# Performance work log

Measured on AMD Instinct MI355X. Metric: run time of the kernel, lower is better.

## Reference

```python
import jax, jax.numpy as jnp
import numpy as np

HID = 512      # hidden_dim
HEADS = 8
DK = HID // HEADS   # 64
WIN = 128      # sliding window (attend to self + previous 128)
TYPE_V = 157
TYPE_D = 192
CONCAT = TYPE_D + 128 + 128 + 128  # 576


def _ln(x, g, b):
    m = jnp.mean(x, -1, keepdims=True)
    v = jnp.mean((x - m) ** 2, -1, keepdims=True)
    return (x - m) * jax.lax.rsqrt(v + 1e-5) * g + b


def _rope(t):
    # interleaved rotary embedding (rotary_embedding_torch default), t: [B,H,L,D]
    d, L = t.shape[-1], t.shape[-2]
    inv = 1.0 / (10000.0 ** (jnp.arange(0, d, 2, dtype=jnp.float32) / d))
    ang = jnp.arange(L, dtype=jnp.float32)[:, None] * inv  # [L, d/2]
    c, s = jnp.cos(ang), jnp.sin(ang)
    x1, x2 = t[..., 0::2], t[..., 1::2]
    return jnp.stack([x1 * c - x2 * s, x1 * s + x2 * c], -1).reshape(t.shape)


def _forward(emb, reg_w, reg_b, br_w, br_b, mem_w, mem_b, inst_w, inst_b,
             ln1_g, ln1_b, qkv_w, outp_w, outp_b, ln2_g, ln2_b, head_w, head_b, x):
    # --- InstructionEncoder ---
    tid = x[..., 0]
    reg = x[..., 1:65].astype(jnp.float32)
    mem = x[..., 65:129].astype(jnp.float32)
    br = x[..., 129:161].astype(jnp.float32)
    cat = jnp.concatenate([
        emb[tid],
        reg @ reg_w.T + reg_b,
        br @ br_w.T + br_b,
        mem @ mem_w.T + mem_b,
    ], -1)
    cat = jax.nn.silu(cat)
    h = jax.nn.silu(_ln(cat @ inst_w.T + inst_b, ln1_g, ln1_b))  # [B,L,HID]

    # --- MultiHeadSelfAttention (banded causal window) ---
    B, L, _ = h.shape
    # torch rearrange '... l (h d c) -> c ... h l d': last dim factors (h, d, 3)
    qkv = (h @ qkv_w.T).reshape(B, L, HEADS, DK, 3)
    q = jnp.transpose(qkv[..., 0], (0, 2, 1, 3))  # [B,H,L,D]
    k = jnp.transpose(qkv[..., 1], (0, 2, 1, 3))
    v = jnp.transpose(qkv[..., 2], (0, 2, 1, 3))
    q = _rope(q)
    k = _rope(k)

    nb = L // WIN
    qb = q.reshape(B, HEADS, nb, WIN, DK)
    kb = k.reshape(B, HEADS, nb, WIN, DK)
    vb = v.reshape(B, HEADS, nb, WIN, DK)
    # each query block attends to its own block and the previous one
    kprev = jnp.pad(kb, ((0, 0), (0, 0), (1, 0), (0, 0), (0, 0)))[:, :, :nb]
    vprev = jnp.pad(vb, ((0, 0), (0, 0), (1, 0), (0, 0), (0, 0)))[:, :, :nb]
    kc = jnp.concatenate([kprev, kb], 3)  # [B,H,nb,2W,D]
    vc = jnp.concatenate([vprev, vb], 3)
    sc = jnp.einsum('bhnqd,bhnkd->bhnqk', qb, kc) / np.sqrt(DK).astype(np.float32)
    qi = jnp.arange(WIN)[:, None]
    kj = jnp.arange(2 * WIN)[None, :]
    rel = (WIN + qi) - kj                      # query_pos - key_pos within band
    allowed = (rel >= 0) & (rel <= WIN)        # causal, window = 128 back
    valid = (kj[None] >= WIN) | (jnp.arange(nb)[:, None, None] > 0)  # no prev block for block 0
    mask = allowed[None] & valid               # [nb, W, 2W]
    sc = jnp.where(mask, sc, jnp.finfo(sc.dtype).min)
    p = jax.nn.softmax(sc, -1)
    o = jnp.einsum('bhnqk,bhnkd->bhnqd', p, vc).reshape(B, HEADS, L, DK)
    o = jnp.transpose(o, (0, 2, 1, 3)).reshape(B, L, HID)
    attn = o @ outp_w.T + outp_b

    # --- MultiTaskOutputHead ---
    y = jax.nn.silu(_ln(attn, ln2_g, ln2_b))
    out = y @ head_w.T + head_b  # [B,L,9]
    fetch = jax.nn.softplus(out[..., 0])
    exec_c = jax.nn.softplus(out[..., 1])
    bm = jax.nn.sigmoid(out[..., 2])
    tlb = jax.nn.sigmoid(out[..., 3])
    ic = jax.nn.sigmoid(out[..., 4])
    dc = jax.nn.softmax(out[..., 5:9], -1)
    return jnp.concatenate([fetch[..., None], exec_c[..., None], bm[..., None],
                            tlb[..., None], ic[..., None], dc], -1)


def setup_inputs():
    key = jax.random.key(0)
    ks = jax.random.split(key, 12)
    B, L = 4, 8192

    def w(k, shape, fan):
        return jax.random.normal(k, shape, jnp.float32) / np.sqrt(fan).astype(np.float32)

    inp = {}
    inp['emb'] = jax.random.normal(ks[0], (TYPE_V, TYPE_D), jnp.float32)
    inp['reg_w'] = w(ks[1], (128, 64), 64); inp['reg_b'] = jnp.zeros((128,), jnp.float32)
    inp['br_w'] = w(ks[2], (128, 32), 32); inp['br_b'] = jnp.zeros((128,), jnp.float32)
    inp['mem_w'] = w(ks[3], (128, 64), 64); inp['mem_b'] = jnp.zeros((128,), jnp.float32)
    inp['inst_w'] = w(ks[4], (HID, CONCAT), CONCAT); inp['inst_b'] = jnp.zeros((HID,), jnp.float32)
    inp['ln1_g'] = jnp.ones((HID,), jnp.float32); inp['ln1_b'] = jnp.zeros((HID,), jnp.float32)
    inp['qkv_w'] = w(ks[5], (3 * HID, HID), HID)
    inp['outp_w'] = w(ks[6], (HID, HID), HID); inp['outp_b'] = jnp.zeros((HID,), jnp.float32)
    inp['ln2_g'] = jnp.ones((HID,), jnp.float32); inp['ln2_b'] = jnp.zeros((HID,), jnp.float32)
    inp['head_w'] = w(ks[7], (9, HID), HID); inp['head_b'] = jnp.zeros((9,), jnp.float32)
    tid = jax.random.randint(ks[8], (B, L, 1), 0, TYPE_V)
    feats = jax.random.randint(ks[9], (B, L, 160), 0, 2)
    inp['x'] = jnp.concatenate([tid, feats], -1).astype(jnp.int32)
    return inp


def reference(emb, reg_w, reg_b, br_w, br_b, mem_w, mem_b, inst_w, inst_b,
              ln1_g, ln1_b, qkv_w, outp_w, outp_b, ln2_g, ln2_b, head_w, head_b, x):
    return _forward(emb, reg_w, reg_b, br_w, br_b, mem_w, mem_b, inst_w, inst_b,
                    ln1_g, ln1_b, qkv_w, outp_w, outp_b, ln2_g, ln2_b, head_w, head_b, x)
```

## Files before the change

### kernel.cpp

```cpp
#include <hip/hip_runtime.h>
#include <hip/hip_bf16.h>
#include <math.h>
#include <type_traits>

#define LSEQ 8192
#define BATCH 4
#define M_TOK (BATCH * LSEQ)

typedef __attribute__((ext_vector_type(8))) short bf16x8;
typedef __attribute__((ext_vector_type(4))) float f32x4;
typedef __attribute__((ext_vector_type(16))) float f32x16;

__device__ __forceinline__ float siluf(float x) {
  return x / (1.f + __expf(-x));
}

__device__ __forceinline__ float bf2f(uint u16) {
  union { float f; uint u; } c;
  c.u = u16 << 16;
  return c.f;
}

__device__ __forceinline__ uint cvtpk_bf16(float lo, float hi) {
  uint r;
  asm volatile("v_cvt_pk_bf16_f32 %0, %1, %2" : "=v"(r) : "v"(lo), "v"(hi));
  return r;
}

__device__ __forceinline__ void perm32swap(uint& a, uint& b) {
  asm volatile("v_permlane32_swap_b32 %0, %1" : "+v"(a), "+v"(b));
}

__device__ __forceinline__ void gload16(const ushort* g, short* l) {
  __builtin_amdgcn_global_load_lds(
      (const __attribute__((address_space(1))) void*)g,
      (__attribute__((address_space(3))) void*)l, 16, 0, 0);
}

#define NW1 (512 * 576)
#define NW3 (512 * 512)
#define NW2 (1536 * 512)
#define NW4 (384 * 192)
#define NTAB (8192 * 32)

__global__ __launch_bounds__(256) void setup_kernel(
    const float* __restrict__ inst_w, const float* __restrict__ outp_w,
    const float* __restrict__ qkv_w, const float* __restrict__ reg_w,
    const float* __restrict__ reg_b, const float* __restrict__ br_w,
    const float* __restrict__ br_b, const float* __restrict__ mem_w,
    const float* __restrict__ mem_b, __hip_bfloat16* __restrict__ w16,
    float2* __restrict__ tab) {
  int i = blockIdx.x * 256 + threadIdx.x;
  if (i < NW1) {
    w16[i] = __float2bfloat16(inst_w[i]);
    return;
  }
  i -= NW1;
  if (i < NW3) {
    w16[NW1 + i] = __float2bfloat16(outp_w[i]);
    return;
  }
  i -= NW3;
  if (i < NW2) {
    int np = i / 512, k = i % 512;
    int which = np >> 9, rem = np & 511;
    int h = rem >> 6, d = rem & 63;
    int n = h * 192 + d * 3 + which;
    w16[NW1 + NW3 + i] = __float2bfloat16(qkv_w[n * 512 + k]);
    return;
  }
  i -= NW2;
  if (i < NW4) {
    int o = i / 192, c = i % 192;
    float v = 0.f;
    if (o < 128) {
      if (c == 0) v = reg_b[o];
      else if (c <= 64) v = reg_w[o * 64 + (c - 1)];
    } else if (o < 256) {
      int oo = o - 128;
      if (c == 0) v = br_b[oo];
      else if (c >= 129 && c <= 160) v = br_w[oo * 32 + (c - 129)];
    } else {
      int oo = o - 256;
      if (c == 0) v = mem_b[oo];
      else if (c >= 65 && c <= 128) v = mem_w[oo * 64 + (c - 65)];
    }
    w16[NW1 + NW3 + NW2 + i] = __float2bfloat16(v);
    return;
  }
  i -= NW4;
  if (i < NTAB) {
    int pos = i >> 5, p = i & 31;
    float inv = expf(-(float)p * 0.28782313662f);
    float sn, cs;
    sincosf((float)pos * inv, &sn, &cs);
    tab[i] = make_float2(cs, sn);
  }
}

__global__ __launch_bounds__(256) void prep_kernel(
    const int* __restrict__ x, const float* __restrict__ emb,
    __hip_bfloat16* __restrict__ cat, __hip_bfloat16* __restrict__ Fb) {
  int gid = blockIdx.x * 256 + threadIdx.x;
  int t = gid / 48;
  int g = gid % 48;
  if (t >= M_TOK) return;
  const int* xr = x + (size_t)t * 161;
  union { __hip_bfloat16 h[8]; uint4 u; } pk;
  if (g < 24) {
    int c0 = g * 8;
    const float* e = emb + xr[0] * 192 + c0;
#pragma unroll
    for (int j = 0; j < 8; ++j) pk.h[j] = __float2bfloat16(siluf(e[j]));
    *(uint4*)&cat[(size_t)t * 576 + c0] = pk.u;
  } else {
    int c0 = (g - 24) * 8;
#pragma unroll
    for (int j = 0; j < 8; ++j) {
      int c = c0 + j;
      float v = (c == 0) ? 1.f : ((c <= 160) ? (float)xr[c] : 0.f);
      pk.h[j] = __float2bfloat16(v);
    }
    *(uint4*)&Fb[(size_t)t * 192 + c0] = pk.u;
  }
}

template <typename OT, bool SILU = false>
__global__ __launch_bounds__(256) void gemm_mfma(
    const ushort* __restrict__ A, const ushort* __restrict__ W,
    const float* __restrict__ bias, OT* __restrict__ C, int M, int N, int K,
    int ldc, int ntn) {
  __shared__ __align__(16) short As[2][128 * 32];
  __shared__ __align__(16) short Bs[2][128 * 32];
  const int tid = threadIdx.x;
  const int lane = tid & 63;
  const int wid = tid >> 6;
  const int wr = wid >> 1, wc = wid & 1;
  const int nwg = gridDim.x;
  const int orig = blockIdx.x;
  const int qq = nwg >> 3, rr = nwg & 7;
  const int xcd = orig & 7;
  const int wgid = (xcd < rr ? xcd * (qq + 1) : rr * (qq + 1) + (xcd - rr) * qq)
                   + (orig >> 3);
  const int row0 = (wgid / ntn) * 128, col0 = (wgid % ntn) * 128;

  const int lrow = lane >> 2;
  const int lch = (lane & 3) * 8;
  const int frow = lane & 15;
  const int fk = (lane >> 4) * 8;

  const ushort* Abase = A + (size_t)(row0 + 32 * wid + lrow) * K + lch;
  const ushort* Wbase = W + (size_t)(col0 + 32 * wid + lrow) * K + lch;
  short* Al[2] = {&As[0][32 * wid * 32], &As[1][32 * wid * 32]};
  short* Bl[2] = {&Bs[0][32 * wid * 32], &Bs[1][32 * wid * 32]};

  f32x4 acc[4][4];
  const f32x4 z = {0.f, 0.f, 0.f, 0.f};
#pragma unroll
  for (int i = 0; i < 4; ++i)
#pragma unroll
    for (int j = 0; j < 4; ++j) acc[i][j] = z;

  const int T = K >> 5;
  gload16(Abase, Al[0]);
  gload16(Abase + (size_t)16 * K, Al[0] + 512);
  gload16(Wbase, Bl[0]);
  gload16(Wbase + (size_t)16 * K, Bl[0] + 512);

  for (int t = 0; t < T; ++t) {
    __syncthreads();
    if (t + 1 < T) {
      const ushort* An = Abase + (t + 1) * 32;
      const ushort* Wn = Wbase + (t + 1) * 32;
      short* Ad = Al[(t + 1) & 1];
      short* Bd = Bl[(t + 1) & 1];
      gload16(An, Ad);
      gload16(An + (size_t)16 * K, Ad + 512);
      gload16(Wn, Bd);
      gload16(Wn + (size_t)16 * K, Bd + 512);
    }
    const short* Ab = As[t & 1];
    const short* Bb = Bs[t & 1];
    bf16x8 af[4], bfr[4];
#pragma unroll
    for (int i = 0; i < 4; ++i)
      af[i] = *(const bf16x8*)&Ab[(wr * 64 + i * 16 + frow) * 32 + fk];
#pragma unroll
    for (int j = 0; j < 4; ++j)
      bfr[j] = *(const bf16x8*)&Bb[(wc * 64 + j * 16 + frow) * 32 + fk];
#pragma unroll
    for (int i = 0; i < 4; ++i)
#pragma unroll
      for (int j = 0; j < 4; ++j)
        acc[i][j] = __builtin_amdgcn_mfma_f32_16x16x32_bf16(af[i], bfr[j],
                                                            acc[i][j], 0, 0, 0);
  }

  const int crow0 = row0 + wr * 64 + (lane >> 4) * 4;
  const int ccol0 = col0 + wc * 64 + (lane & 15);
#pragma unroll
  for (int j = 0; j < 4; ++j) {
    const int col = ccol0 + j * 16;
    const float bv = bias ? bias[col] : 0.f;
#pragma unroll
    for (int i = 0; i < 4; ++i) {
#pragma unroll
      for (int r = 0; r < 4; ++r) {
        float v = acc[i][j][r] + bv;
        if constexpr (SILU) v = siluf(v);
        size_t off = (size_t)(crow0 + i * 16 + r) * ldc + col;
        if constexpr (std::is_same<OT, float>::value) {
          C[off] = v;
        } else {
          C[off] = __float2bfloat16(v);
        }
      }
    }
  }
}

template <bool HEAD>
__global__ __launch_bounds__(512, 2) void gemm_ln_fused(
    const ushort* __restrict__ A, const ushort* __restrict__ W,
    const float* __restrict__ bias, const float* __restrict__ g,
    const float* __restrict__ b2, const float* __restrict__ hw,
    const float* __restrict__ hb, __hip_bfloat16* __restrict__ C,
    float* __restrict__ out, int K) {
  __shared__ __align__(16) short As[2][128 * 32];
  __shared__ __align__(16) short Bs[2][512 * 32];
  __shared__ float rs[4][128], rss[4][128];
  __shared__ float o9[4][128][9];
  const int tid = threadIdx.x;
  const int lane = tid & 63;
  const int wid = tid >> 6;
  const int wr = wid & 1, wc = wid >> 1;
  const int row0 = blockIdx.x * 128;
  const int frow = lane & 15;
  const int fk = (lane >> 4) * 8;

  const ushort* Abase =
      A + (size_t)(row0 + 16 * wid + (lane >> 2)) * K + (lane & 3) * 8;
  const ushort* Wbase = W + (size_t)(64 * wid + (lane >> 2)) * K + (lane & 3) * 8;
  short* Adst[2] = {&As[0][16 * wid * 32], &As[1][16 * wid * 32]};
  short* Bdst[2] = {&Bs[0][64 * wid * 32], &Bs[1][64 * wid * 32]};

  f32x4 acc[4][8];
  const f32x4 z = {0.f, 0.f, 0.f, 0.f};
#pragma unroll
  for (int i = 0; i < 4; ++i)
#pragma unroll
    for (int j = 0; j < 8; ++j) acc[i][j] = z;

  const int T = K >> 5;
  gload16(Abase, Adst[0]);
#pragma unroll
  for (int q = 0; q < 4; ++q)
    gload16(Wbase + (size_t)q * 16 * K, Bdst[0] + q * 16 * 32);

  for (int t = 0; t < T; ++t) {
    __syncthreads();
    if (t + 1 < T) {
      const ushort* An = Abase + (t + 1) * 32;
      const ushort* Wn = Wbase + (t + 1) * 32;
      short* Ad = Adst[(t + 1) & 1];
      short* Bd = Bdst[(t + 1) & 1];
      gload16(An, Ad);
#pragma unroll
      for (int q = 0; q < 4; ++q)
        gload16(Wn + (size_t)q * 16 * K, Bd + q * 16 * 32);
    }
    const short* Ab = As[t & 1];
    const short* Bb = Bs[t & 1];
    bf16x8 af[4], bfr[8];
#pragma unroll
    for (int i = 0; i < 4; ++i)
      af[i] = *(const bf16x8*)&Ab[(wr * 64 + i * 16 + frow) * 32 + fk];
#pragma unroll
    for (int j = 0; j < 8; ++j)
      bfr[j] = *(const bf16x8*)&Bb[(wc * 128 + j * 16 + frow) * 32 + fk];
#pragma unroll
    for (int i = 0; i < 4; ++i)
#pragma unroll
      for (int j = 0; j < 8; ++j)
        acc[i][j] = __builtin_amdgcn_mfma_f32_16x16x32_bf16(af[i], bfr[j],
                                                            acc[i][j], 0, 0, 0);
  }

  float bv[8], gv[8], b2v[8];
#pragma unroll
  for (int j = 0; j < 8; ++j) {
    int col = wc * 128 + (lane & 15) + j * 16;
    bv[j] = bias[col];
    gv[j] = g[col];
    b2v[j] = b2[col];
  }
  float sum_[4][4], sq_[4][4];
#pragma unroll
  for (int i = 0; i < 4; ++i)
#pragma unroll
    for (int r = 0; r < 4; ++r) { sum_[i][r] = 0.f; sq_[i][r] = 0.f; }
#pragma unroll
  for (int i = 0; i < 4; ++i)
#pragma unroll
    for (int j = 0; j < 8; ++j)
#pragma unroll
      for (int r = 0; r < 4; ++r) {
        float v = acc[i][j][r] + bv[j];
        acc[i][j][r] = v;
        sum_[i][r] += v;
        sq_[i][r] += v * v;
      }
#pragma unroll
  for (int i = 0; i < 4; ++i)
#pragma unroll
    for (int r = 0; r < 4; ++r)
#pragma unroll
      for (int off = 1; off < 16; off <<= 1) {
        sum_[i][r] += __shfl_xor(sum_[i][r], off, 64);
        sq_[i][r] += __shfl_xor(sq_[i][r], off, 64);
      }
  if ((lane & 15) == 0) {
#pragma unroll
    for (int i = 0; i < 4; ++i)
#pragma unroll
      for (int r = 0; r < 4; ++r) {
        int lr = wr * 64 + (lane >> 4) * 4 + i * 16 + r;
        rs[wc][lr] = sum_[i][r];
        rss[wc][lr] = sq_[i][r];
      }
  }
  __syncthreads();
#pragma unroll
  for (int i = 0; i < 4; ++i)
#pragma unroll
    for (int r = 0; r < 4; ++r) {
      int lr = wr * 64 + (lane >> 4) * 4 + i * 16 + r;
      float S = rs[0][lr] + rs[1][lr] + rs[2][lr] + rs[3][lr];
      float SS = rss[0][lr] + rss[1][lr] + rss[2][lr] + rss[3][lr];
      float mean = S * (1.f / 512.f);
      float var = SS * (1.f / 512.f) - mean * mean;
      float rstd = rsqrtf(var + 1e-5f);
#pragma unroll
      for (int j = 0; j < 8; ++j) {
        float y = (acc[i][j][r] - mean) * rstd * gv[j] + b2v[j];
        acc[i][j][r] = siluf(y);
      }
    }

  if constexpr (!HEAD) {
#pragma unroll
    for (int i = 0; i < 4; ++i)
#pragma unroll
      for (int r = 0; r < 4; ++r) {
        int grow = row0 + wr * 64 + (lane >> 4) * 4 + i * 16 + r;
#pragma unroll
        for (int j = 0; j < 8; ++j)
          C[(size_t)grow * 512 + wc * 128 + (lane & 15) + j * 16] =
              __float2bfloat16(acc[i][j][r]);
      }
  } else {
#pragma unroll
    for (int r9 = 0; r9 < 9; ++r9) {
      float hw8[8];
#pragma unroll
      for (int j = 0; j < 8; ++j)
        hw8[j] = hw[r9 * 512 + wc * 128 + (lane & 15) + j * 16];
      float pacc[4][4];
#pragma unroll
      for (int i = 0; i < 4; ++i)
#pragma unroll
        for (int r = 0; r < 4; ++r) {
          float p = 0.f;
#pragma unroll
          for (int j = 0; j < 8; ++j) p = fmaf(acc[i][j][r], hw8[j], p);
#pragma unroll
          for (int off = 1; off < 16; off <<= 1) p += __shfl_xor(p, off, 64);
          pacc[i][r] = p;
        }
      if ((lane & 15) == 0) {
#pragma unroll
        for (int i = 0; i < 4; ++i)
#pragma unroll
          for (int r = 0; r < 4; ++r) {
            int lr = wr * 64 + (lane >> 4) * 4 + i * 16 + r;
            o9[wc][lr][r9] = pacc[i][r];
          }
      }
    }
    __syncthreads();
    if (tid < 128) {
      float raw[9];
#pragma unroll
      for (int r9 = 0; r9 < 9; ++r9)
        raw[r9] = o9[0][tid][r9] + o9[1][tid][r9] + o9[2][tid][r9] +
                  o9[3][tid][r9] + hb[r9];
      float* op = out + (size_t)(row0 + tid) * 9;
      op[0] = fmaxf(raw[0], 0.f) + log1pf(expf(-fabsf(raw[0])));
      op[1] = fmaxf(raw[1], 0.f) + log1pf(expf(-fabsf(raw[1])));
      op[2] = 1.f / (1.f + expf(-raw[2]));
      op[3] = 1.f / (1.f + expf(-raw[3]));
      op[4] = 1.f / (1.f + expf(-raw[4]));
      float mx = fmaxf(fmaxf(raw[5], raw[6]), fmaxf(raw[7], raw[8]));
      float e0 = expf(raw[5] - mx), e1 = expf(raw[6] - mx);
      float e2 = expf(raw[7] - mx), e3 = expf(raw[8] - mx);
      float inv = 1.f / (e0 + e1 + e2 + e3);
      op[5] = e0 * inv; op[6] = e1 * inv; op[7] = e2 * inv; op[8] = e3 * inv;
    }
  }
}

__global__ __launch_bounds__(256) void attn_kernel(
    const __hip_bfloat16* __restrict__ qkv, const float2* __restrict__ tab,
    __hip_bfloat16* __restrict__ o_out) {
  __shared__ __align__(16) short Kc[2][64 * 72];
  __shared__ __align__(16) short Vt[2][64 * 72];
  __shared__ __align__(16) float rbuf[4][32];
  const int blk = blockIdx.x;
  const int nbIdx = blk & 63;
  const int h = (blk >> 6) & 7;
  const int b = blk >> 9;
  const int tid = threadIdx.x;
  const int w = tid >> 6;
  const int lane = tid & 63;
  const int lq = lane & 31;
  const int hi = lane >> 5;
  const size_t seqBase = (size_t)b * LSEQ;
  const int qi = w * 32 + lq;
  const int qtok = nbIdx * 128 + qi;

  const ushort* qkvu = (const ushort*)qkv;

  bf16x8 qf[4];
  {
    const ushort* Qrow = qkvu + (seqBase + qtok) * 1536 + h * 64;
#pragma unroll
    for (int s = 0; s < 4; ++s) {
      int dim0 = 16 * s + 8 * hi;
      bf16x8 qv = *(const bf16x8*)(Qrow + dim0);
      const float4* tp = (const float4*)(tab + qtok * 32 + dim0 / 2);
      float4 t01 = tp[0], t23 = tp[1];
      float cs[4] = {t01.x, t01.z, t23.x, t23.z};
      float sn[4] = {t01.y, t01.w, t23.y, t23.w};
      union { uint u[4]; bf16x8 v; } pk;
#pragma unroll
      for (int j = 0; j < 4; ++j) {
        float x1 = bf2f((ushort)qv[2 * j]);
        float x2 = bf2f((ushort)qv[2 * j + 1]);
        float r0 = (x1 * cs[j] - x2 * sn[j]) * 0.125f;
        float r1 = (x1 * sn[j] + x2 * cs[j]) * 0.125f;
        pk.u[j] = cvtpk_bf16(r0, r1);
      }
      qf[s] = pk.v;
    }
  }

  const f32x16 Z16 = {0.f};
  f32x16 oa0 = Z16, oa1 = Z16;
  float m0 = -3.0e38f, l = 0.f;

  const int cstart = (nbIdx == 0) ? 2 : 0;
  const int cw0 = (w >= 2) ? 1 : 0;
  const int cw1 = (w >= 2) ? 3 : 2;

  const int skk = tid >> 2;
  const int sd0 = (tid & 3) * 16;

  bf16x8 kreg0, kreg1, vreg0, vreg1;

  auto issue = [&](int c) {
    int ktok = (nbIdx - 1) * 128 + c * 64 + skk;
    const ushort* base = qkvu + (seqBase + ktok) * 1536 + h * 64 + sd0;
    kreg0 = *(const bf16x8*)(base + 512);
    kreg1 = *(const bf16x8*)(base + 512 + 8);
    vreg0 = *(const bf16x8*)(base + 1024);
    vreg1 = *(const bf16x8*)(base + 1024 + 8);
  };

  auto write_chunk = [&](int c) {
    short* Kb = Kc[c & 1];
    short* Vb = Vt[c & 1];
    int ktok = (nbIdx - 1) * 128 + c * 64 + skk;
    const float4* tp = (const float4*)(tab + ktok * 32 + (sd0 >> 1));
    float4 t0 = tp[0], t1 = tp[1], t2 = tp[2], t3 = tp[3];
    const int swk = ((skk >> 3) & 3) << 5;
    {
      float cs[4] = {t0.x, t0.z, t1.x, t1.z};
      float sn[4] = {t0.y, t0.w, t1.y, t1.w};
      union { uint u[4]; bf16x8 v; } pk;
#pragma unroll
      for (int j = 0; j < 4; ++j) {
        float x1 = bf2f((ushort)kreg0[2 * j]);
        float x2 = bf2f((ushort)kreg0[2 * j + 1]);
        pk.u[j] = cvtpk_bf16(x1 * cs[j] - x2 * sn[j], x1 * sn[j] + x2 * cs[j]);
      }
      *(bf16x8*)((char*)Kb + skk * 144 + ((sd0 * 2) ^ swk)) = pk.v;
    }
    {
      float cs[4] = {t2.x, t2.z, t3.x, t3.z};
      float sn[4] = {t2.y, t2.w, t3.y, t3.w};
      union { uint u[4]; bf16x8 v; } pk;
#pragma unroll
      for (int j = 0; j < 4; ++j) {
        float x1 = bf2f((ushort)kreg1[2 * j]);
        float x2 = bf2f((ushort)kreg1[2 * j + 1]);
        pk.u[j] = cvtpk_bf16(x1 * cs[j] - x2 * sn[j], x1 * sn[j] + x2 * cs[j]);
      }
      *(bf16x8*)((char*)Kb + skk * 144 + (((sd0 + 8) * 2) ^ swk)) = pk.v;
    }
#pragma unroll
    for (int j = 0; j < 8; ++j) {
      int d0 = sd0 + j;
      *(short*)((char*)Vb + d0 * 144 +
                ((skk * 2) ^ (((d0 >> 4) & 3) << 5))) = vreg0[j];
      int d1 = sd0 + 8 + j;
      *(short*)((char*)Vb + d1 * 144 +
                ((skk * 2) ^ (((d1 >> 4) & 3) << 5))) = vreg1[j];
    }
  };

  issue(cstart);
  write_chunk(cstart);

  for (int c = cstart; c < 4; ++c) {
    if (c < 3) issue(c + 1);
    __syncthreads();
    if (c >= cw0 && c <= cw1) {
      const char* Kb = (const char*)Kc[c & 1];
      const char* Vb = (const char*)Vt[c & 1];

      bf16x8 ka[2][4];
#pragma unroll
      for (int t2 = 0; t2 < 2; ++t2)
#pragma unroll
        for (int s = 0; s < 4; ++s) {
          int kk = 32 * t2 + lq;
          int byteoff =
              kk * 144 + ((32 * s + 16 * hi) ^ (((kk >> 3) & 3) << 5));
          ka[t2][s] = *(const bf16x8*)(Kb + byteoff);
        }
      f32x16 st0 = Z16, st1 = Z16;
#pragma unroll
      for (int s = 0; s < 4; ++s) {
        st0 = __builtin_amdgcn_mfma_f32_32x32x16_bf16(ka[0][s], qf[s], st0, 0, 0, 0);
        st1 = __builtin_amdgcn_mfma_f32_32x32x16_bf16(ka[1][s], qf[s], st1, 0, 0, 0);
      }

      float p2[2][16];
      float pmax = -3.0e38f;
#pragma unroll
      for (int t2 = 0; t2 < 2; ++t2)
#pragma unroll
        for (int r = 0; r < 16; ++r) {
          int key = c * 64 + 32 * t2 + (r & 3) + 8 * (r >> 2) + 4 * hi;
          float sv = (t2 ? st1[r] : st0[r]);
          bool act = (key >= qi) && (key <= qi + 128);
          sv = act ? sv : -1.0e30f;
          p2[t2][r] = sv;
          pmax = fmaxf(pmax, sv);
        }
      pmax = fmaxf(pmax, __shfl_xor(pmax, 32));
      if (__any(pmax > m0 + 8.f)) {
        float nm = fmaxf(m0, pmax);
        float rr2 = __expf(m0 - nm);
        l *= rr2;
        m0 = nm;
        rbuf[w][lq] = rr2;
        asm volatile("s_waitcnt lgkmcnt(0)" ::: "memory");
#pragma unroll
        for (int a = 0; a < 4; ++a) {
          f32x4 r4 = *(const f32x4*)&rbuf[w][8 * a + 4 * hi];
#pragma unroll
          for (int j = 0; j < 4; ++j) {
            oa0[4 * a + j] *= r4[j];
            oa1[4 * a + j] *= r4[j];
          }
        }
      }
      float lsum = 0.f;
#pragma unroll
      for (int t2 = 0; t2 < 2; ++t2)
#pragma unroll
        for (int r = 0; r < 16; ++r) {
          float p = __expf(p2[t2][r] - m0);
          p2[t2][r] = p;
          lsum += p;
        }
      l += lsum + __shfl_xor(lsum, 32);

      union { uint u[4]; bf16x8 v; } pa[4];
#pragma unroll
      for (int t2 = 0; t2 < 2; ++t2)
#pragma unroll
        for (int sl = 0; sl < 2; ++sl) {
          const float* pp = &p2[t2][8 * sl];
          uint a0 = cvtpk_bf16(pp[0], pp[1]);
          uint a1 = cvtpk_bf16(pp[2], pp[3]);
          uint b0 = cvtpk_bf16(pp[4], pp[5]);
          uint b1 = cvtpk_bf16(pp[6], pp[7]);
          perm32swap(a0, b0);
          perm32swap(a1, b1);
          int slot = 2 * t2 + sl;
          pa[slot].u[0] = a0; pa[slot].u[1] = a1;
          pa[slot].u[2] = b0; pa[slot].u[3] = b1;
        }

#pragma unroll
      for (int slot = 0; slot < 4; ++slot) {
        {
          int d = lq;
          int byteoff =
              d * 144 + ((32 * slot + 16 * hi) ^ (((d >> 4) & 3) << 5));
          bf16x8 vb = *(const bf16x8*)(Vb + byteoff);
          oa0 = __builtin_amdgcn_mfma_f32_32x32x16_bf16(pa[slot].v, vb, oa0, 0, 0, 0);
        }
        {
          int d = 32 + lq;
          int byteoff =
              d * 144 + ((32 * slot + 16 * hi) ^ (((d >> 4) & 3) << 5));
          bf16x8 vb = *(const bf16x8*)(Vb + byteoff);
          oa1 = __builtin_amdgcn_mfma_f32_32x32x16_bf16(pa[slot].v, vb, oa1, 0, 0, 0);
        }
      }
    }
    if (c < 3) write_chunk(c + 1);
  }

  rbuf[w][lq] = 1.f / l;
  asm volatile("s_waitcnt lgkmcnt(0)" ::: "memory");
  const int q0 = nbIdx * 128 + 32 * w;
#pragma unroll
  for (int a = 0; a < 4; ++a) {
    f32x4 r4 = *(const f32x4*)&rbuf[w][8 * a + 4 * hi];
#pragma unroll
    for (int j = 0; j < 4; ++j) {
      int tok = q0 + 8 * a + 4 * hi + j;
      __hip_bfloat16* orow = o_out + (seqBase + tok) * 512 + h * 64;
      orow[lq] = __float2bfloat16(oa0[4 * a + j] * r4[j]);
      orow[32 + lq] = __float2bfloat16(oa1[4 * a + j] * r4[j]);
    }
  }
}

extern "C" void kernel_launch(void* const* d_in, const int* in_sizes, int n_in,
                              void* d_out, int out_size, void* d_ws,
                              size_t ws_size, hipStream_t stream) {
  const float* emb = (const float*)d_in[0];
  const float* reg_w = (const float*)d_in[1];
  const float* reg_b = (const float*)d_in[2];
  const float* br_w = (const float*)d_in[3];
  const float* br_b = (const float*)d_in[4];
  const float* mem_w = (const float*)d_in[5];
  const float* mem_b = (const float*)d_in[6];
  const float* inst_w = (const float*)d_in[7];
  const float* inst_b = (const float*)d_in[8];
  const float* ln1_g = (const float*)d_in[9];
  const float* ln1_b = (const float*)d_in[10];
  const float* qkv_w = (const float*)d_in[11];
  const float* outp_w = (const float*)d_in[12];
  const float* outp_b = (const float*)d_in[13];
  const float* ln2_g = (const float*)d_in[14];
  const float* ln2_b = (const float*)d_in[15];
  const float* head_w = (const float*)d_in[16];
  const float* head_b = (const float*)d_in[17];
  const int* x = (const int*)d_in[18];
  float* out = (float*)d_out;

  const int M = M_TOK;
  char* wsb = (char*)d_ws;
  __hip_bfloat16* w16 = (__hip_bfloat16*)wsb;
  __hip_bfloat16* w1 = w16;
  __hip_bfloat16* w3 = w16 + NW1;
  __hip_bfloat16* w2 = w16 + NW1 + NW3;
  __hip_bfloat16* wcat = w16 + NW1 + NW3 + NW2;
  size_t woff = ((size_t)(NW1 + NW2 + NW3 + NW4) * 2 + 255) & ~(size_t)255;
  float2* tab = (float2*)(wsb + woff);
  size_t toff = woff + (size_t)NTAB * 8;
  char* r1 = wsb + toff;
  char* r2 = r1 + (size_t)M * 1536 * 2;
  __hip_bfloat16* cat = (__hip_bfloat16*)r1;
  __hip_bfloat16* Fb = (__hip_bfloat16*)(r1 + (size_t)M * 576 * 2);
  __hip_bfloat16* qkvb = (__hip_bfloat16*)r1;
  __hip_bfloat16* hb = (__hip_bfloat16*)r2;
  __hip_bfloat16* att = (__hip_bfloat16*)r2;

  const int setup_tot = NW1 + NW3 + NW2 + NW4 + NTAB;
  setup_kernel<<<(setup_tot + 255) / 256, 256, 0, stream>>>(
      inst_w, outp_w, qkv_w, reg_w, reg_b, br_w, br_b, mem_w, mem_b, w16, tab);
  prep_kernel<<<(M * 48) / 256, 256, 0, stream>>>(x, emb, cat, Fb);
  gemm_mfma<__hip_bfloat16, true><<<(M / 128) * 3, 256, 0, stream>>>(
      (const ushort*)Fb, (const ushort*)wcat, nullptr, cat + 192, M, 384, 192,
      576, 3);
  gemm_ln_fused<false><<<M / 128, 512, 0, stream>>>(
      (const ushort*)cat, (const ushort*)w1, inst_b, ln1_g, ln1_b, nullptr,
      nullptr, hb, nullptr, 576);
  gemm_mfma<__hip_bfloat16><<<(M / 128) * 12, 256, 0, stream>>>(
      (const ushort*)hb, (const ushort*)w2, nullptr, qkvb, M, 1536, 512, 1536,
      12);
  attn_kernel<<<BATCH * 8 * 64, 256, 0, stream>>>(qkvb, tab, att);
  gemm_ln_fused<true><<<M / 128, 512, 0, stream>>>(
      (const ushort*)att, (const ushort*)w3, outp_b, ln2_g, ln2_b, head_w,
      head_b, nullptr, out, 512);
}
```

Baseline: 255.9 us.

## Add 256x256-tile QKV GEMM with 4-stage async pipeline and XCD-aware block remap

Replaces the generic 128-tile GEMM for the QKV projection with a dedicated kernel that uses 256x256 output tiles across 8 waves. It adds a 4-deep shared-memory ring of direct global-to-LDS loads with explicit vmcnt waits, a swizzled LDS layout, s_setprio around the MFMA block, and a remap of block IDs so neighbouring tiles land on the same XCD. The goal is more operand reuse per load and better latency hiding for this large GEMM. The cost is 128KB of LDS per block, which may limit occupancy, plus hand-written wait counts that must match the load issue order exactly.

Measured after the change: 261.6 us. +2.2%, slower.

```diff
diff --git a/kernel.cpp b/kernel.cpp
--- a/kernel.cpp
+++ b/kernel.cpp
@@ -214,6 +214,108 @@
         } else {
           C[off] = __float2bfloat16(v);
         }
+      }
+    }
+  }
+}
+
+__global__ __launch_bounds__(512, 2) void gemm_qkv8(
+    const ushort* __restrict__ A, const ushort* __restrict__ W,
+    __hip_bfloat16* __restrict__ C, int ldc, int ntn) {
+  __shared__ __align__(16) short LA[4][8192];
+  __shared__ __align__(16) short LB[4][8192];
+  const int tid = threadIdx.x;
+  const int lane = tid & 63;
+  const int wid = tid >> 6;
+  const int wm = wid >> 2;
+  const int wn = wid & 3;
+  const int nwg = gridDim.x;
+  const int orig = blockIdx.x;
+  const int qq = nwg >> 3, rr = nwg & 7;
+  const int xcd = orig & 7;
+  const int wgid = (xcd < rr ? xcd * (qq + 1) : rr * (qq + 1) + (xcd - rr) * qq)
+                   + (orig >> 3);
+  const int row0 = (wgid / ntn) * 256, col0 = (wgid % ntn) * 256;
+
+  const int l2 = lane >> 2;
+  const int swch = ((lane & 3) ^ (l2 & 3)) << 3;
+  const int arow = wid * 16 + l2;
+  const ushort* A0 = A + (size_t)(row0 + arow) * 512 + swch;
+  const ushort* A1 = A0 + (size_t)128 * 512;
+  const ushort* B0 = W + (size_t)(col0 + arow) * 512 + swch;
+  const ushort* B1 = B0 + (size_t)128 * 512;
+
+  f32x4 acc[8][4];
+  const f32x4 z = {0.f, 0.f, 0.f, 0.f};
+#pragma unroll
+  for (int i = 0; i < 8; ++i)
+#pragma unroll
+    for (int j = 0; j < 4; ++j) acc[i][j] = z;
+
+  auto stage = [&](int kt, int b) {
+    gload16(A0 + kt * 32, &LA[b][wid * 512]);
+    gload16(A1 + kt * 32, &LA[b][4096 + wid * 512]);
+    gload16(B0 + kt * 32, &LB[b][wid * 512]);
+    gload16(B1 + kt * 32, &LB[b][4096 + wid * 512]);
+  };
+
+  const int fr = lane & 15;
+  const int cg = lane >> 4;
+
+  auto compute = [&](int kt) {
+    const short* Ab = LA[kt & 3];
+    const short* Bb = LB[kt & 3];
+    bf16x8 af[8], bfr[4];
+#pragma unroll
+    for (int i = 0; i < 8; ++i) {
+      int row = wm * 128 + i * 16 + fr;
+      af[i] = *(const bf16x8*)&Ab[row * 32 + ((cg ^ (row & 3)) << 3)];
+    }
+#pragma unroll
+    for (int j = 0; j < 4; ++j) {
+      int row = wn * 64 + j * 16 + fr;
+      bfr[j] = *(const bf16x8*)&Bb[row * 32 + ((cg ^ (row & 3)) << 3)];
+    }
+    __builtin_amdgcn_s_setprio(1);
+#pragma unroll
+    for (int i = 0; i < 8; ++i)
+#pragma unroll
+      for (int j = 0; j < 4; ++j)
+        acc[i][j] = __builtin_amdgcn_mfma_f32_16x16x32_bf16(af[i], bfr[j],
+                                                            acc[i][j], 0, 0, 0);
+    __builtin_amdgcn_s_setprio(0);
+  };
+
+  stage(0, 0);
+  stage(1, 1);
+  stage(2, 2);
+
+  for (int kt = 0; kt < 16; ++kt) {
+    asm volatile("s_barrier" ::: "memory");
+    if (kt < 13) {
+      stage(kt + 3, (kt + 3) & 3);
+      asm volatile("s_waitcnt vmcnt(12)" ::: "memory");
+    } else if (kt == 13) {
+      asm volatile("s_waitcnt vmcnt(8)" ::: "memory");
+    } else if (kt == 14) {
+      asm volatile("s_waitcnt vmcnt(4)" ::: "memory");
+    } else {
+      asm volatile("s_waitcnt vmcnt(0)" ::: "memory");
+    }
+    asm volatile("s_barrier" ::: "memory");
+    compute(kt);
+  }
+
+  const int crow0 = row0 + wm * 128 + (lane >> 4) * 4;
+  const int ccol0 = col0 + wn * 64 + (lane & 15);
+#pragma unroll
+  for (int i = 0; i < 8; ++i) {
+#pragma unroll
+    for (int j = 0; j < 4; ++j) {
+#pragma unroll
+      for (int r = 0; r < 4; ++r) {
+        size_t off = (size_t)(crow0 + i * 16 + r) * ldc + ccol0 + j * 16;
+        C[off] = __float2bfloat16(acc[i][j][r]);
       }
     }
   }
@@ -693,9 +795,8 @@
   gemm_ln_fused<false><<<M / 128, 512, 0, stream>>>(
       (const ushort*)cat, (const ushort*)w1, inst_b, ln1_g, ln1_b, nullptr,
       nullptr, hb, nullptr, 576);
-  gemm_mfma<__hip_bfloat16><<<(M / 128) * 12, 256, 0, stream>>>(
-      (const ushort*)hb, (const ushort*)w2, nullptr, qkvb, M, 1536, 512, 1536,
-      12);
+  gemm_qkv8<<<(M / 256) * (1536 / 256), 512, 0, stream>>>(
+      (const ushort*)hb, (const ushort*)w2, qkvb, 1536, 1536 / 256);
   attn_kernel<<<BATCH * 8 * 64, 256, 0, stream>>>(qkvb, tab, att);
   gemm_ln_fused<true><<<M / 128, 512, 0, stream>>>(
       (const ushort*)att, (const ushort*)w3, outp_b, ln2_g, ln2_b, head_w,
```
